# Kernel tuning notes

Hardware: AMD Instinct MI355X
Metric: run time of the kernel (lower is better)

## Reference

```python
import jax, jax.numpy as jnp
import numpy as np

N, IN_F, E, EDGE_F, H, C = 50000, 128, 800000, 32, 4, 32
NEG_SLOPE = 0.2
EPS = 1e-16


def setup_inputs() -> dict:
    key = jax.random.key(0)
    ks = jax.random.split(key, 10)
    s = lambda *sh: 1.0 / np.sqrt(sh[-1])
    return {
        "node_features": jax.random.normal(ks[0], (N, IN_F), jnp.float32),
        "edge_features": jax.random.normal(ks[1], (E, EDGE_F), jnp.float32),
        "edge_index": jax.random.randint(ks[2], (2, E), 0, N, jnp.int32),
        # GATConv params
        "W_gat": jax.random.normal(ks[3], (H * C, IN_F), jnp.float32) * s(IN_F),
        "att_src": jax.random.normal(ks[4], (H, C), jnp.float32) * s(C),
        "att_dst": jax.random.normal(ks[5], (H, C), jnp.float32) * s(C),
        "att_edge": jax.random.normal(ks[6], (H, C), jnp.float32) * s(C),
        "bias": jnp.zeros((H * C,), jnp.float32),
        # edge_linear and skip_connection weights
        "W_edge": jax.random.normal(ks[7], (H * C, EDGE_F), jnp.float32) * s(EDGE_F),
        "W_skip": jax.random.normal(ks[8], (H * C, IN_F), jnp.float32) * s(IN_F),
    }


def reference(node_features, edge_features, edge_index, W_gat, att_src, att_dst,
              att_edge, bias, W_edge, W_skip):
    src, dst = edge_index[0], edge_index[1]
    # edge_linear + view(-1, H, C)
    e_attr = (edge_features @ W_edge.T).reshape(E, H, C)
    # GATConv: per-head linear transform of nodes -> [N, H, C]
    x = (node_features @ W_gat.T).reshape(N, H, C)
    # attention logits: a_src.x_i + a_dst.x_j + a_edge.e  -> [E, H]
    a_src = jnp.einsum('nhc,hc->nh', x, att_src)
    a_dst = jnp.einsum('nhc,hc->nh', x, att_dst)
    a_edge = jnp.einsum('ehc,hc->eh', e_attr, att_edge)
    alpha = jax.nn.leaky_relu(a_src[src] + a_dst[dst] + a_edge, NEG_SLOPE)
    # segment softmax over incoming edges of each destination node
    m = jax.ops.segment_max(alpha, dst, num_segments=N)  # [N, H]
    m = jnp.where(jnp.isfinite(m), m, 0.0)
    ex = jnp.exp(alpha - m[dst])
    denom = jax.ops.segment_sum(ex, dst, num_segments=N)  # [N, H]
    attn = ex / (denom[dst] + EPS)  # [E, H]
    # message = alpha * x_src ; scatter-add to destination
    msg = x[src] * attn[:, :, None]  # [E, H, C]
    out = jax.ops.segment_sum(msg, dst, num_segments=N)  # [N, H, C]
    out = out.reshape(N, H * C) + bias  # concat=True
    # skip connection + ELU activation
    out = out + node_features @ W_skip.T
    return jax.nn.elu(out)
```

## Files before the change

kernel.cpp:

```cpp
#include <hip/hip_runtime.h>
#include <hip/hip_bf16.h>

constexpr int N_NODES = 50000;
constexpr int IN_F    = 128;
constexpr long E_EDGES = 800000;
constexpr int EDGE_F  = 32;
constexpr int H_HEADS = 4;
constexpr int C_CH    = 32;
constexpr int HC      = 128;
constexpr float NEG_SLOPE = 0.2f;
constexpr float EPS = 1e-16f;
constexpr int CPAD = 16;
constexpr int NB_SCAN = (N_NODES + 255) / 256;
constexpr int NB_EL   = (int)(E_EDGES / 256);
constexpr int NB_HIST4 = (int)((E_EDGES + 1023) / 1024);
constexpr int NB_AE2  = (int)(E_EDGES / 128);
constexpr int NB_ZEROP = (int)((N_NODES * CPAD + 255) / 256);
constexpr float SM_SHIFT = 12.0f;

typedef __attribute__((ext_vector_type(8))) short bf16x8;
typedef __attribute__((ext_vector_type(4))) float f32x4;

__device__ __forceinline__ unsigned short f2b(float f) {
    __hip_bfloat16 h = __float2bfloat16(f);
    return *reinterpret_cast<unsigned short*>(&h);
}
__device__ __forceinline__ float b2f_lo(unsigned v) { return __uint_as_float(v << 16); }
__device__ __forceinline__ float b2f_hi(unsigned v) { return __uint_as_float(v & 0xffff0000u); }

__global__ __launch_bounds__(256) void setup_kernel(
    const float* __restrict__ Wg, const float* __restrict__ Ws,
    unsigned short* __restrict__ wcat, const float* __restrict__ We,
    const float* __restrict__ att_edge, float* __restrict__ weff,
    int* __restrict__ counts)
{
    const int b = blockIdx.x, t = threadIdx.x;
    if (b < 32) {
        int i = (b * 256 + t) * 4;
        const float* srcp = (i < 16384) ? (Wg + i) : (Ws + i - 16384);
        float4 v = *(const float4*)srcp;
        ushort4 o;
        o.x = f2b(v.x); o.y = f2b(v.y); o.z = f2b(v.z); o.w = f2b(v.w);
        *(ushort4*)&wcat[i] = o;
    } else if (b == 32) {
        if (t < 128) {
            int h = t >> 5, f = t & 31;
            float acc = 0.f;
#pragma unroll
            for (int c = 0; c < C_CH; ++c)
                acc = fmaf(We[(h * C_CH + c) * EDGE_F + f], att_edge[h * C_CH + c], acc);
            weff[t] = acc;
        }
    } else {
        int i = (b - 33) * 256 + t;
        if (i < N_NODES * CPAD) counts[i] = 0;
    }
}

__global__ __launch_bounds__(256) void hist_kernel(
    const int* __restrict__ dst, int* __restrict__ counts,
    int* __restrict__ rank)
{
    long e0 = (long)blockIdx.x * 1024 + threadIdx.x * 4;
    if (e0 + 3 < E_EDGES) {
        int4 d4 = *(const int4*)(dst + e0);
        int4 r4;
        r4.x = atomicAdd(&counts[d4.x * CPAD], 1);
        r4.y = atomicAdd(&counts[d4.y * CPAD], 1);
        r4.z = atomicAdd(&counts[d4.z * CPAD], 1);
        r4.w = atomicAdd(&counts[d4.w * CPAD], 1);
        *(int4*)(rank + e0) = r4;
    } else {
        for (long e = e0; e < E_EDGES; ++e)
            rank[e] = atomicAdd(&counts[dst[e] * CPAD], 1);
    }
}

__global__ __launch_bounds__(256) void ae_kernel(
    const float* __restrict__ ef, const float* __restrict__ weff,
    float* __restrict__ ae)
{
    const int t = threadIdx.x;
    const int l = t & 63, wv = t >> 6;
    const int sub = l & 3, eIdx = l >> 2;
    const long eb = (long)blockIdx.x * 128 + wv * 32 + eIdx;
    const float4* ef4 = (const float4*)ef;

    float4 a0 = ef4[eb * 8 + sub];
    float4 b0 = ef4[eb * 8 + 4 + sub];
    float4 a1 = ef4[(eb + 16) * 8 + sub];
    float4 b1 = ef4[(eb + 16) * 8 + 4 + sub];

    const float4* wf4 = (const float4*)weff;
    float4 wa[4], wb[4];
#pragma unroll
    for (int h = 0; h < 4; ++h) { wa[h] = wf4[h * 8 + sub]; wb[h] = wf4[h * 8 + 4 + sub]; }

    float p[4];
#pragma unroll
    for (int h = 0; h < 4; ++h) {
        float acc = 0.f;
        acc = fmaf(a0.x, wa[h].x, acc); acc = fmaf(a0.y, wa[h].y, acc);
        acc = fmaf(a0.z, wa[h].z, acc); acc = fmaf(a0.w, wa[h].w, acc);
        acc = fmaf(b0.x, wb[h].x, acc); acc = fmaf(b0.y, wb[h].y, acc);
        acc = fmaf(b0.z, wb[h].z, acc); acc = fmaf(b0.w, wb[h].w, acc);
        p[h] = acc;
    }
#pragma unroll
    for (int h = 0; h < 4; ++h) {
        p[h] += __shfl_xor(p[h], 1);
        p[h] += __shfl_xor(p[h], 2);
    }
    float v0 = (sub == 0) ? p[0] : (sub == 1) ? p[1] : (sub == 2) ? p[2] : p[3];
    ae[eb * 4 + sub] = v0;

#pragma unroll
    for (int h = 0; h < 4; ++h) {
        float acc = 0.f;
        acc = fmaf(a1.x, wa[h].x, acc); acc = fmaf(a1.y, wa[h].y, acc);
        acc = fmaf(a1.z, wa[h].z, acc); acc = fmaf(a1.w, wa[h].w, acc);
        acc = fmaf(b1.x, wb[h].x, acc); acc = fmaf(b1.y, wb[h].y, acc);
        acc = fmaf(b1.z, wb[h].z, acc); acc = fmaf(b1.w, wb[h].w, acc);
        p[h] = acc;
    }
#pragma unroll
    for (int h = 0; h < 4; ++h) {
        p[h] += __shfl_xor(p[h], 1);
        p[h] += __shfl_xor(p[h], 2);
    }
    float v1 = (sub == 0) ? p[0] : (sub == 1) ? p[1] : (sub == 2) ? p[2] : p[3];
    ae[(eb + 16) * 4 + sub] = v1;
}

__global__ __launch_bounds__(256) void mfma_gemm_kernel(
    const float* __restrict__ nf, const unsigned short* __restrict__ wcat,
    const float* __restrict__ bias, unsigned short* __restrict__ xb,
    float* __restrict__ out)
{
    const int t  = threadIdx.x;
    const int w  = t >> 6;
    const int l  = t & 63;
    const int lr = l & 15;
    const int lk = l >> 4;
    const int n0 = blockIdx.x * 64;

    bf16x8 bfr[4][4];
#pragma unroll
    for (int nfr = 0; nfr < 4; ++nfr)
#pragma unroll
        for (int ks = 0; ks < 4; ++ks)
            bfr[nfr][ks] = *(const bf16x8*)&wcat[(w * 64 + nfr * 16 + lr) * 128 + ks * 32 + lk * 8];

    f32x4 acc[4][4];
#pragma unroll
    for (int mf = 0; mf < 4; ++mf)
#pragma unroll
        for (int nfr = 0; nfr < 4; ++nfr)
            acc[mf][nfr] = (f32x4){0.f, 0.f, 0.f, 0.f};

#pragma unroll
    for (int ks = 0; ks < 4; ++ks) {
        bf16x8 afr[4];
#pragma unroll
        for (int mf = 0; mf < 4; ++mf) {
            int row = n0 + mf * 16 + lr;
            row = row < N_NODES ? row : N_NODES - 1;
            const float* ap = nf + (size_t)row * IN_F + ks * 32 + lk * 8;
            float4 a0 = *(const float4*)ap;
            float4 a1 = *(const float4*)(ap + 4);
            bf16x8 f;
            f[0] = (short)f2b(a0.x); f[1] = (short)f2b(a0.y);
            f[2] = (short)f2b(a0.z); f[3] = (short)f2b(a0.w);
            f[4] = (short)f2b(a1.x); f[5] = (short)f2b(a1.y);
            f[6] = (short)f2b(a1.z); f[7] = (short)f2b(a1.w);
            afr[mf] = f;
        }
#pragma unroll
        for (int mf = 0; mf < 4; ++mf)
#pragma unroll
            for (int nfr = 0; nfr < 4; ++nfr)
                acc[mf][nfr] = __builtin_amdgcn_mfma_f32_16x16x32_bf16(
                    afr[mf], bfr[nfr][ks], acc[mf][nfr], 0, 0, 0);
    }

#pragma unroll
    for (int nfr = 0; nfr < 4; ++nfr) {
        const int gc = w * 64 + nfr * 16 + lr;
        if (gc < HC) {
#pragma unroll
            for (int mf = 0; mf < 4; ++mf)
#pragma unroll
                for (int r = 0; r < 4; ++r) {
                    int m = n0 + mf * 16 + lk * 4 + r;
                    if (m < N_NODES) xb[(size_t)m * HC + gc] = f2b(acc[mf][nfr][r]);
                }
        } else {
            const float bv = bias[gc - HC];
#pragma unroll
            for (int mf = 0; mf < 4; ++mf)
#pragma unroll
                for (int r = 0; r < 4; ++r) {
                    int m = n0 + mf * 16 + lk * 4 + r;
                    if (m < N_NODES) out[(size_t)m * HC + gc - HC] = acc[mf][nfr][r] + bv;
                }
        }
    }
}

__global__ __launch_bounds__(256) void a_kernel(
    const unsigned int* __restrict__ xb32, const float* __restrict__ att_src,
    const float* __restrict__ att_dst, float* __restrict__ asrc,
    float* __restrict__ adst)
{
    const int wave = threadIdx.x >> 6, lane = threadIdx.x & 63;
    const int n = blockIdx.x * 4 + wave;
    if (n >= N_NODES) return;
    unsigned v = xb32[(size_t)n * 64 + lane];
    float x0 = b2f_lo(v), x1 = b2f_hi(v);
    float2 as = ((const float2*)att_src)[lane];
    float2 ad = ((const float2*)att_dst)[lane];
    float ps = x0 * as.x + x1 * as.y;
    float pd = x0 * ad.x + x1 * ad.y;
#pragma unroll
    for (int off = 1; off < 16; off <<= 1) {
        ps += __shfl_xor(ps, off);
        pd += __shfl_xor(pd, off);
    }
    if ((lane & 15) == 0) {
        asrc[(size_t)n * H_HEADS + (lane >> 4)] = ps;
        adst[(size_t)n * H_HEADS + (lane >> 4)] = pd;
    }
}

__global__ __launch_bounds__(256) void scan1_kernel(const int* __restrict__ counts,
                                                    int* __restrict__ row_ptr,
                                                    int* __restrict__ blocksum)
{
    __shared__ int s[256];
    int t = threadIdx.x;
    int i = blockIdx.x * 256 + t;
    int v = (i < N_NODES) ? counts[i * CPAD] : 0;
    s[t] = v;
    __syncthreads();
#pragma unroll
    for (int off = 1; off < 256; off <<= 1) {
        int u = (t >= off) ? s[t - off] : 0;
        __syncthreads();
        s[t] += u;
        __syncthreads();
    }
    if (i < N_NODES) row_ptr[i] = s[t] - v;
    if (t == 255) blocksum[blockIdx.x] = s[255];
}

__global__ __launch_bounds__(256) void scan2_kernel(int* __restrict__ blocksum)
{
    __shared__ int s[256];
    int t = threadIdx.x;
    int v = (t < NB_SCAN) ? blocksum[t] : 0;
    s[t] = v;
    __syncthreads();
#pragma unroll
    for (int off = 1; off < 256; off <<= 1) {
        int u = (t >= off) ? s[t - off] : 0;
        __syncthreads();
        s[t] += u;
        __syncthreads();
    }
    blocksum[t] = s[t] - v;
}

__global__ __launch_bounds__(256) void scan3_kernel(int* __restrict__ row_ptr,
                                                    const int* __restrict__ blocksum)
{
    int i = blockIdx.x * 256 + threadIdx.x;
    if (i < N_NODES) row_ptr[i] = row_ptr[i] + blocksum[blockIdx.x];
    if (i == 0) row_ptr[N_NODES] = (int)E_EDGES;
}

__global__ __launch_bounds__(256) void edge_logits_kernel(
    const int* __restrict__ src, const int* __restrict__ dst,
    const float* __restrict__ ae, const float* __restrict__ asrc,
    const float* __restrict__ adst, const int* __restrict__ row_ptr,
    const int* __restrict__ rank, uint4* __restrict__ rec4)
{
    const long e = (long)blockIdx.x * 256 + threadIdx.x;

    const int s  = src[e];
    const int d  = dst[e];
    const int rk = rank[e];
    float4 a_e = ((const float4*)ae)[e];

    float4 as4 = ((const float4*)asrc)[s];
    float4 ad4 = ((const float4*)adst)[d];
    const int pos = row_ptr[d] + rk;

    float lg[4] = {as4.x + ad4.x + a_e.x, as4.y + ad4.y + a_e.y,
                   as4.z + ad4.z + a_e.z, as4.w + ad4.w + a_e.w};
    uint4 r;
    unsigned* rw = (unsigned*)&r;
#pragma unroll
    for (int h = 0; h < 4; ++h) {
        float al = lg[h] > 0.f ? lg[h] : NEG_SLOPE * lg[h];
        rw[h] = (__float_as_uint(al) & 0xFFFFFF00u)
              | ((unsigned)(s >> (8 * h)) & 0xFFu);
    }
    rec4[pos] = r;
}

__device__ __forceinline__ void accum8(float* acc, uint4 v, float e) {
    acc[0] = fmaf(b2f_lo(v.x), e, acc[0]);
    acc[1] = fmaf(b2f_hi(v.x), e, acc[1]);
    acc[2] = fmaf(b2f_lo(v.y), e, acc[2]);
    acc[3] = fmaf(b2f_hi(v.y), e, acc[3]);
    acc[4] = fmaf(b2f_lo(v.z), e, acc[4]);
    acc[5] = fmaf(b2f_hi(v.z), e, acc[5]);
    acc[6] = fmaf(b2f_lo(v.w), e, acc[6]);
    acc[7] = fmaf(b2f_hi(v.w), e, acc[7]);
}

__device__ __forceinline__ int rec_src(uint4 r) {
    return (int)((r.x & 0xFFu) | ((r.y & 0xFFu) << 8));
}
__device__ __forceinline__ float rec_alpha(uint4 r, int h) {
    unsigned w = h == 0 ? r.x : h == 1 ? r.y : h == 2 ? r.z : r.w;
    return __uint_as_float(w & 0xFFFFFF00u);
}

__global__ __launch_bounds__(256) void aggregate_kernel(
    const int* __restrict__ row_ptr, const uint4* __restrict__ rec4,
    const uint4* __restrict__ xb4, float* __restrict__ out)
{
    const int wave = threadIdx.x >> 6;
    const int lane = threadIdx.x & 63;
    const int d = blockIdx.x * 4 + wave;
    if (d >= N_NODES) return;
    const int beg = row_ptr[d], end = row_ptr[d + 1];
    const int q  = lane >> 4;
    const int cg = lane & 15;
    const int h  = cg >> 2;

    float acc[8] = {0.f, 0.f, 0.f, 0.f, 0.f, 0.f, 0.f, 0.f};
    float dsum = 0.f;

    int i = beg;
    for (; i + 8 <= end; i += 8) {
        int i0 = i + q, i1 = i + 4 + q;
        uint4 r0 = rec4[i0];
        uint4 r1 = rec4[i1];
        int s0 = rec_src(r0);
        int s1 = rec_src(r1);
        float a0 = rec_alpha(r0, h);
        float a1 = rec_alpha(r1, h);
        uint4 v0 = xb4[(size_t)s0 * 16 + cg];
        uint4 v1 = xb4[(size_t)s1 * 16 + cg];
        float e0 = __expf(a0 - SM_SHIFT);
        float e1 = __expf(a1 - SM_SHIFT);
        dsum += e0 + e1;
        accum8(acc, v0, e0);
        accum8(acc, v1, e1);
    }
    for (; i < end; i += 4) {
        int idx = i + q;
        bool val = idx < end;
        int ii = val ? idx : end - 1;
        uint4 r = rec4[ii];
        int s = rec_src(r);
        float a = rec_alpha(r, h);
        uint4 v = xb4[(size_t)s * 16 + cg];
        float e = val ? __expf(a - SM_SHIFT) : 0.f;
        dsum += e;
        accum8(acc, v, e);
    }

#pragma unroll
    for (int off = 16; off <= 32; off <<= 1) {
        dsum += __shfl_xor(dsum, off);
#pragma unroll
        for (int k = 0; k < 8; ++k) acc[k] += __shfl_xor(acc[k], off);
    }
    const float inv = 1.f / (dsum + EPS);

    if (q == 0) {
        float* op = out + (size_t)d * HC + cg * 8;
        float4 o0 = *(const float4*)op;
        float4 o1 = *(const float4*)(op + 4);
        o0.x += acc[0] * inv; o0.y += acc[1] * inv;
        o0.z += acc[2] * inv; o0.w += acc[3] * inv;
        o1.x += acc[4] * inv; o1.y += acc[5] * inv;
        o1.z += acc[6] * inv; o1.w += acc[7] * inv;
        o0.x = o0.x > 0.f ? o0.x : expf(o0.x) - 1.f;
        o0.y = o0.y > 0.f ? o0.y : expf(o0.y) - 1.f;
        o0.z = o0.z > 0.f ? o0.z : expf(o0.z) - 1.f;
        o0.w = o0.w > 0.f ? o0.w : expf(o0.w) - 1.f;
        o1.x = o1.x > 0.f ? o1.x : expf(o1.x) - 1.f;
        o1.y = o1.y > 0.f ? o1.y : expf(o1.y) - 1.f;
        o1.z = o1.z > 0.f ? o1.z : expf(o1.z) - 1.f;
        o1.w = o1.w > 0.f ? o1.w : expf(o1.w) - 1.f;
        *(float4*)op = o0;
        *(float4*)(op + 4) = o1;
    }
}

extern "C" void kernel_launch(void* const* d_in, const int* in_sizes, int n_in,
                              void* d_out, int out_size, void* d_ws, size_t ws_size,
                              hipStream_t stream)
{
    const float* nf       = (const float*)d_in[0];
    const float* ef       = (const float*)d_in[1];
    const int*   ei       = (const int*)d_in[2];
    const float* Wg       = (const float*)d_in[3];
    const float* att_src  = (const float*)d_in[4];
    const float* att_dst  = (const float*)d_in[5];
    const float* att_edge = (const float*)d_in[6];
    const float* bias     = (const float*)d_in[7];
    const float* We       = (const float*)d_in[8];
    const float* Ws       = (const float*)d_in[9];
    float* out = (float*)d_out;

    const int* src = ei;
    const int* dst = ei + E_EDGES;

    unsigned int* rec   = (unsigned int*)d_ws;
    float* ae           = (float*)(rec + 4 * E_EDGES);
    unsigned short* xb  = (unsigned short*)(ae + 4 * E_EDGES);
    unsigned short* wcat= xb + (size_t)N_NODES * HC;
    float* asrc         = (float*)(wcat + 256 * 128);
    float* adst         = asrc + (size_t)N_NODES * H_HEADS;
    float* weff         = adst + (size_t)N_NODES * H_HEADS;
    int*   counts       = (int*)(weff + 128);
    int*   row_ptr      = counts + (size_t)N_NODES * CPAD;
    int*   blocksum     = row_ptr + N_NODES + 1;
    int*   rank         = blocksum + 256;

    setup_kernel<<<33 + NB_ZEROP, 256, 0, stream>>>(
        Wg, Ws, wcat, We, att_edge, weff, counts);
    hist_kernel<<<NB_HIST4, 256, 0, stream>>>(dst, counts, rank);
    ae_kernel<<<NB_AE2, 256, 0, stream>>>(ef, weff, ae);
    mfma_gemm_kernel<<<(N_NODES + 63) / 64, 256, 0, stream>>>(
        nf, wcat, bias, xb, out);
    a_kernel<<<(N_NODES + 3) / 4, 256, 0, stream>>>(
        (const unsigned int*)xb, att_src, att_dst, asrc, adst);
    scan1_kernel<<<NB_SCAN, 256, 0, stream>>>(counts, row_ptr, blocksum);
    scan2_kernel<<<1, 256, 0, stream>>>(blocksum);
    scan3_kernel<<<NB_SCAN, 256, 0, stream>>>(row_ptr, blocksum);
    edge_logits_kernel<<<NB_EL, 256, 0, stream>>>(
        src, dst, ae, asrc, adst, row_ptr, rank, (uint4*)rec);
    aggregate_kernel<<<(N_NODES + 3) / 4, 256, 0, stream>>>(
        row_ptr, (const uint4*)rec, (const uint4*)xb, out);
}
```

Before: 175.7 us.

## Replace global atomic histogram with per-block LDS histograms for CSR build

Builds the destination histogram with 64 blocks, each holding a packed 16-bit-per-node histogram in LDS (100KB), instead of global atomics on padded counters. Per-block histograms are reduced in scan1 and expanded into per-block offsets in scan3, so edge_logits computes positions from block offset plus a 16-bit local rank. This removes the zeroing of the padded counter array and the contended global atomics. In exchange, only 64 blocks do the histogram, and scan3 writes a 64xN offset table (about 12.8MB) that edge_logits then reads at random.

```diff
diff --git a/kernel.cpp b/kernel.cpp
--- a/kernel.cpp
+++ b/kernel.cpp
@@ -10,12 +10,12 @@
 constexpr int HC      = 128;
 constexpr float NEG_SLOPE = 0.2f;
 constexpr float EPS = 1e-16f;
-constexpr int CPAD = 16;
+constexpr int B_HIST = 64;
+constexpr int CHUNK  = (int)(E_EDGES / B_HIST);
+constexpr int HWORDS = N_NODES / 2;
 constexpr int NB_SCAN = (N_NODES + 255) / 256;
 constexpr int NB_EL   = (int)(E_EDGES / 256);
-constexpr int NB_HIST4 = (int)((E_EDGES + 1023) / 1024);
 constexpr int NB_AE2  = (int)(E_EDGES / 128);
-constexpr int NB_ZEROP = (int)((N_NODES * CPAD + 255) / 256);
 constexpr float SM_SHIFT = 12.0f;
 
 typedef __attribute__((ext_vector_type(8))) short bf16x8;
@@ -31,8 +31,7 @@
 __global__ __launch_bounds__(256) void setup_kernel(
     const float* __restrict__ Wg, const float* __restrict__ Ws,
     unsigned short* __restrict__ wcat, const float* __restrict__ We,
-    const float* __restrict__ att_edge, float* __restrict__ weff,
-    int* __restrict__ counts)
+    const float* __restrict__ att_edge, float* __restrict__ weff)
 {
     const int b = blockIdx.x, t = threadIdx.x;
     if (b < 32) {
@@ -42,7 +41,7 @@
         ushort4 o;
         o.x = f2b(v.x); o.y = f2b(v.y); o.z = f2b(v.z); o.w = f2b(v.w);
         *(ushort4*)&wcat[i] = o;
-    } else if (b == 32) {
+    } else {
         if (t < 128) {
             int h = t >> 5, f = t & 31;
             float acc = 0.f;
@@ -51,29 +50,27 @@
                 acc = fmaf(We[(h * C_CH + c) * EDGE_F + f], att_edge[h * C_CH + c], acc);
             weff[t] = acc;
         }
-    } else {
-        int i = (b - 33) * 256 + t;
-        if (i < N_NODES * CPAD) counts[i] = 0;
     }
 }
 
 __global__ __launch_bounds__(256) void hist_kernel(
-    const int* __restrict__ dst, int* __restrict__ counts,
-    int* __restrict__ rank)
-{
-    long e0 = (long)blockIdx.x * 1024 + threadIdx.x * 4;
-    if (e0 + 3 < E_EDGES) {
-        int4 d4 = *(const int4*)(dst + e0);
-        int4 r4;
-        r4.x = atomicAdd(&counts[d4.x * CPAD], 1);
-        r4.y = atomicAdd(&counts[d4.y * CPAD], 1);
-        r4.z = atomicAdd(&counts[d4.z * CPAD], 1);
-        r4.w = atomicAdd(&counts[d4.w * CPAD], 1);
-        *(int4*)(rank + e0) = r4;
-    } else {
-        for (long e = e0; e < E_EDGES; ++e)
-            rank[e] = atomicAdd(&counts[dst[e] * CPAD], 1);
-    }
+    const int* __restrict__ dst, unsigned int* __restrict__ histB,
+    unsigned short* __restrict__ rank16)
+{
+    __shared__ unsigned int h[HWORDS];
+    const int t = threadIdx.x, b = blockIdx.x;
+    for (int i = t; i < HWORDS; i += 256) h[i] = 0;
+    __syncthreads();
+    const int e0 = b * CHUNK;
+    for (int i = t; i < CHUNK; i += 256) {
+        int d = dst[e0 + i];
+        int sh = (d & 1) * 16;
+        unsigned old = atomicAdd(&h[d >> 1], 1u << sh);
+        rank16[e0 + i] = (unsigned short)((old >> sh) & 0xFFFFu);
+    }
+    __syncthreads();
+    unsigned int* outp = histB + (size_t)b * HWORDS;
+    for (int i = t; i < HWORDS; i += 256) outp[i] = h[i];
 }
 
 __global__ __launch_bounds__(256) void ae_kernel(
@@ -232,14 +229,20 @@
     }
 }
 
-__global__ __launch_bounds__(256) void scan1_kernel(const int* __restrict__ counts,
+__global__ __launch_bounds__(256) void scan1_kernel(const unsigned int* __restrict__ histB,
                                                     int* __restrict__ row_ptr,
                                                     int* __restrict__ blocksum)
 {
     __shared__ int s[256];
     int t = threadIdx.x;
     int i = blockIdx.x * 256 + t;
-    int v = (i < N_NODES) ? counts[i * CPAD] : 0;
+    int v = 0;
+    if (i < N_NODES) {
+        int w = i >> 1, sh = (i & 1) * 16;
+#pragma unroll 8
+        for (int b = 0; b < B_HIST; ++b)
+            v += (int)((histB[(size_t)b * HWORDS + w] >> sh) & 0xFFFFu);
+    }
     s[t] = v;
     __syncthreads();
 #pragma unroll
@@ -271,29 +274,41 @@
 }
 
 __global__ __launch_bounds__(256) void scan3_kernel(int* __restrict__ row_ptr,
-                                                    const int* __restrict__ blocksum)
+                                                    const int* __restrict__ blocksum,
+                                                    const unsigned int* __restrict__ histB,
+                                                    int* __restrict__ off)
 {
     int i = blockIdx.x * 256 + threadIdx.x;
-    if (i < N_NODES) row_ptr[i] = row_ptr[i] + blocksum[blockIdx.x];
+    if (i < N_NODES) {
+        int run = row_ptr[i] + blocksum[blockIdx.x];
+        row_ptr[i] = run;
+        int w = i >> 1, sh = (i & 1) * 16;
+#pragma unroll 8
+        for (int b = 0; b < B_HIST; ++b) {
+            off[(size_t)b * N_NODES + i] = run;
+            run += (int)((histB[(size_t)b * HWORDS + w] >> sh) & 0xFFFFu);
+        }
+    }
     if (i == 0) row_ptr[N_NODES] = (int)E_EDGES;
 }
 
 __global__ __launch_bounds__(256) void edge_logits_kernel(
     const int* __restrict__ src, const int* __restrict__ dst,
     const float* __restrict__ ae, const float* __restrict__ asrc,
-    const float* __restrict__ adst, const int* __restrict__ row_ptr,
-    const int* __restrict__ rank, uint4* __restrict__ rec4)
-{
-    const long e = (long)blockIdx.x * 256 + threadIdx.x;
+    const float* __restrict__ adst, const int* __restrict__ off,
+    const unsigned short* __restrict__ rank16, uint4* __restrict__ rec4)
+{
+    const int e = blockIdx.x * 256 + threadIdx.x;
 
     const int s  = src[e];
     const int d  = dst[e];
-    const int rk = rank[e];
+    const int rk = (int)rank16[e];
     float4 a_e = ((const float4*)ae)[e];
 
     float4 as4 = ((const float4*)asrc)[s];
     float4 ad4 = ((const float4*)adst)[d];
-    const int pos = row_ptr[d] + rk;
+    const int be = e / CHUNK;
+    const int pos = off[(size_t)be * N_NODES + d] + rk;
 
     float lg[4] = {as4.x + ad4.x + a_e.x, as4.y + ad4.y + a_e.y,
                    as4.z + ad4.z + a_e.z, as4.w + ad4.w + a_e.w};
@@ -428,24 +443,25 @@
     float* asrc         = (float*)(wcat + 256 * 128);
     float* adst         = asrc + (size_t)N_NODES * H_HEADS;
     float* weff         = adst + (size_t)N_NODES * H_HEADS;
-    int*   counts       = (int*)(weff + 128);
-    int*   row_ptr      = counts + (size_t)N_NODES * CPAD;
+    unsigned int* histB = (unsigned int*)(weff + 128);
+    int*   off          = (int*)(histB + (size_t)B_HIST * HWORDS);
+    int*   row_ptr      = off + (size_t)B_HIST * N_NODES;
     int*   blocksum     = row_ptr + N_NODES + 1;
-    int*   rank         = blocksum + 256;
-
-    setup_kernel<<<33 + NB_ZEROP, 256, 0, stream>>>(
-        Wg, Ws, wcat, We, att_edge, weff, counts);
-    hist_kernel<<<NB_HIST4, 256, 0, stream>>>(dst, counts, rank);
+    unsigned short* rank16 = (unsigned short*)(blocksum + 256);
+
+    setup_kernel<<<33, 256, 0, stream>>>(
+        Wg, Ws, wcat, We, att_edge, weff);
+    hist_kernel<<<B_HIST, 256, 0, stream>>>(dst, histB, rank16);
     ae_kernel<<<NB_AE2, 256, 0, stream>>>(ef, weff, ae);
     mfma_gemm_kernel<<<(N_NODES + 63) / 64, 256, 0, stream>>>(
         nf, wcat, bias, xb, out);
     a_kernel<<<(N_NODES + 3) / 4, 256, 0, stream>>>(
         (const unsigned int*)xb, att_src, att_dst, asrc, adst);
-    scan1_kernel<<<NB_SCAN, 256, 0, stream>>>(counts, row_ptr, blocksum);
+    scan1_kernel<<<NB_SCAN, 256, 0, stream>>>(histB, row_ptr, blocksum);
     scan2_kernel<<<1, 256, 0, stream>>>(blocksum);
-    scan3_kernel<<<NB_SCAN, 256, 0, stream>>>(row_ptr, blocksum);
+    scan3_kernel<<<NB_SCAN, 256, 0, stream>>>(row_ptr, blocksum, histB, off);
     edge_logits_kernel<<<NB_EL, 256, 0, stream>>>(
-        src, dst, ae, asrc, adst, row_ptr, rank, (uint4*)rec);
+        src, dst, ae, asrc, adst, off, rank16, (uint4*)rec);
     aggregate_kernel<<<(N_NODES + 3) / 4, 256, 0, stream>>>(
         row_ptr, (const uint4*)rec, (const uint4*)xb, out);
 }
```

Result: no change. 174.9 us (-0.4%).
